# Performance work log

Hardware: AMD Instinct MI355X
Metric: run time of the kernel (lower is better)

## Reference

```python
import jax, jax.numpy as jnp
import numpy as np

G, P = 128, 32          # num scenes, peds per scene
H, E = 64, 64           # h_dim, embedding_dim_pooling
D1, D2 = 512, 1024      # mlp_pre_pool dims
EPS = 1e-5


def setup_inputs() -> dict:
    key = jax.random.key(0)
    ks = jax.random.split(key, 16)
    N = G * P
    starts = jnp.arange(G, dtype=jnp.int64) * P
    seq_start_end = jnp.stack([starts, starts + P], axis=1)
    def lin(k, fin, fout):
        kw, kb = jax.random.split(k)
        s = 1.0 / np.sqrt(fin)
        return (jax.random.uniform(kw, (fin, fout), jnp.float32, -s, s),
                jax.random.uniform(kb, (fout,), jnp.float32, -s, s))
    Ws, bs = lin(ks[0], 2, E)
    Wv, bv = lin(ks[1], 1, E)
    W1, b1 = lin(ks[2], 3 * E, D1)
    W2, b2 = lin(ks[3], D1, D2)
    return {
        "h_states": jax.random.normal(ks[4], (N, H), jnp.float32),
        "seq_start_end": seq_start_end,
        "end_pos": jax.random.normal(ks[5], (N, 2), jnp.float32),
        "end_pos_speed": jax.random.uniform(ks[6], (N, 1), jnp.float32),
        "Ws": Ws, "bs": bs, "Wv": Wv, "bv": bv,
        "W1": W1, "b1": b1, "g1": jnp.ones((D1,), jnp.float32), "be1": jnp.zeros((D1,), jnp.float32),
        "W2": W2, "b2": b2, "g2": jnp.ones((D2,), jnp.float32), "be2": jnp.zeros((D2,), jnp.float32),
    }


def _bn(h, gamma, beta):
    # BatchNorm1d in train mode, stats over the per-group edge batch (axes 1,2)
    m = h.mean(axis=(1, 2), keepdims=True)
    v = ((h - m) ** 2).mean(axis=(1, 2), keepdims=True)  # biased variance
    return (h - m) * jax.lax.rsqrt(v + EPS) * gamma + beta


def reference(h_states, seq_start_end, end_pos, end_pos_speed,
              Ws, bs, Wv, bv, W1, b1, g1, be1, W2, b2, g2, be2):
    g = seq_start_end.shape[0]
    p = h_states.shape[0] // g
    pos = end_pos.reshape(g, p, 2)
    spd = end_pos_speed.reshape(g, p, 1)
    hid = h_states.reshape(g, p, H)
    # edge (i, j): rel = pos[j] - pos[i]; features of j for hidden & speed
    rel = pos[:, None, :, :] - pos[:, :, None, :]          # [G,P(i),P(j),2]
    rel_e = rel @ Ws + bs                                   # [G,P,P,E]
    spd_e = spd @ Wv + bv                                   # [G,P,E]
    hid_b = jnp.broadcast_to(hid[:, None, :, :], (g, p, p, H))
    spd_b = jnp.broadcast_to(spd_e[:, None, :, :], (g, p, p, E))
    x = jnp.concatenate([rel_e, hid_b, spd_b], axis=-1)     # [G,P,P,3E]
    h1 = jax.nn.relu(_bn(x @ W1 + b1, g1, be1))             # [G,P,P,512]
    h2 = jax.nn.relu(_bn(h1 @ W2 + b2, g2, be2))            # [G,P,P,1024]
    pooled = h2.max(axis=2)                                 # max over j
    return pooled.reshape(g * p, -1)
```

## Files before the change

kernel.cpp:

```cpp
#include <hip/hip_runtime.h>
#include <cstdint>

typedef unsigned short ushort_t;
typedef __attribute__((ext_vector_type(8))) __bf16 bf16x8;
typedef __attribute__((ext_vector_type(4))) float f32x4;
typedef __attribute__((ext_vector_type(4))) int i32x4;

#define NG 128
#define NP 32
#define NH 64
#define ND1 512
#define ND2 1024

__device__ inline ushort_t f2bf(float f) {
    uint32_t u = __float_as_uint(f);
    uint32_t r = (u + 0x7FFFu + ((u >> 16) & 1u)) >> 16;
    return (ushort_t)r;
}

#define GLL16(gp, lp) __builtin_amdgcn_global_load_lds( \
    (const __attribute__((address_space(1))) unsigned int*)(gp), \
    (__attribute__((address_space(3))) unsigned int*)(lp), 16, 0, 0)

__global__ void k2_all(const float* __restrict__ hstates, const float* __restrict__ pos,
                       const float* __restrict__ spd, const float* __restrict__ W1,
                       const float* __restrict__ g1, const float* __restrict__ be1,
                       const float* __restrict__ Ws, const float* __restrict__ bs,
                       const float* __restrict__ Wv, const float* __restrict__ bv,
                       const float* __restrict__ b1, const float* __restrict__ W2,
                       ushort_t* __restrict__ W2T,
                       float* __restrict__ u1, float* __restrict__ w1,
                       float* __restrict__ psum) {
    __shared__ float hid_s[32][64];
    __shared__ float pos_s[32][2];
    __shared__ float spd_s[32];
    __shared__ ushort_t tile[64][65];
    int b = blockIdx.x, tid = threadIdx.x;
    if (b < 256) {
        int t0 = b * 256 + tid;
        #pragma unroll
        for (int z = 0; z < 4; z++) psum[t0 + z * 65536] = 0.f;
        int g = b >> 1;
        int ch = ((b & 1) << 8) + tid;
        for (int t = tid; t < 2048; t += 256) hid_s[t >> 6][t & 63] = hstates[g * 2048 + t];
        if (tid < 64) pos_s[tid >> 1][tid & 1] = pos[g * 64 + tid];
        if (tid < 32) spd_s[tid] = spd[g * 32 + tid];
        float m0 = 0.f, m1 = 0.f, uu = 0.f, vv = b1[ch];
        for (int e = 0; e < 64; e++) {
            float w1a = W1[e * ND1 + ch];
            float w1c = W1[(128 + e) * ND1 + ch];
            m0 += Ws[e] * w1a;
            m1 += Ws[64 + e] * w1a;
            uu += Wv[e] * w1c;
            vv += bs[e] * w1a + bv[e] * w1c;
        }
        __syncthreads();
        float cj[32], qj[32];
        #pragma unroll
        for (int j = 0; j < 32; j++) {
            qj[j] = pos_s[j][0] * m0 + pos_s[j][1] * m1;
            cj[j] = vv + spd_s[j] * uu;
        }
        for (int h = 0; h < 64; h++) {
            float w = W1[(64 + h) * ND1 + ch];
            #pragma unroll
            for (int j = 0; j < 32; j++) cj[j] += hid_s[j][h] * w;
        }
        float S1 = 0.f, S2 = 0.f, C1 = 0.f, Cq = 0.f, C2 = 0.f;
        #pragma unroll
        for (int j = 0; j < 32; j++) {
            S1 += qj[j]; S2 += qj[j] * qj[j];
            C1 += cj[j]; Cq += cj[j] * qj[j]; C2 += cj[j] * cj[j];
        }
        float mean = C1 * (1.0f / 32.0f);
        float sumsq = 64.f * S2 - 2.f * S1 * S1 + 64.f * Cq - 2.f * S1 * C1 + 32.f * C2;
        float var = sumsq * (1.0f / 1024.0f) - mean * mean;
        float A1 = rsqrtf(var + 1e-5f) * g1[ch];
        float B1 = be1[ch] - mean * A1;
        #pragma unroll
        for (int j = 0; j < 32; j++) {
            u1[(g * 32 + j) * ND1 + ch] = (qj[j] + cj[j]) * A1 + B1;
            w1[(g * 32 + j) * ND1 + ch] = qj[j] * A1;
        }
    } else {
        int tb = b - 256;
        int kb2 = tb & 7, nb = tb >> 3;
        #pragma unroll
        for (int e = 0; e < 16; e++) {
            int lin = tid + e * 256;
            int k = lin >> 6, n = lin & 63;
            tile[k][n] = f2bf(W2[(kb2 * 64 + k) * ND2 + nb * 64 + n]);
        }
        __syncthreads();
        #pragma unroll
        for (int e = 0; e < 16; e++) {
            int lin = tid + e * 256;
            int kl = lin & 63, nl = lin >> 6;
            int n = nb * 64 + nl, k = kb2 * 64 + kl;
            int idx = n * ND1 + ((k >> 6) << 6) + (((((k >> 3) & 7) ^ (n & 7))) << 3) + (k & 7);
            W2T[idx] = tile[kl][nl];
        }
    }
}

__global__ void k2b_h1(const float* __restrict__ u1c, const float* __restrict__ w1c,
                       ushort_t* __restrict__ h1) {
    int t = blockIdx.x * 256 + threadIdx.x;
    int k8 = t & 63;
    int row = t >> 6;
    int gc = row >> 10, rem = row & 1023;
    int i = rem >> 5, j = rem & 31;
    const float4* pu = reinterpret_cast<const float4*>(u1c + (size_t)(gc * 32 + j) * ND1 + k8 * 8);
    const float4* pw = reinterpret_cast<const float4*>(w1c + (size_t)(gc * 32 + i) * ND1 + k8 * 8);
    float4 ua = pu[0], ub = pu[1], wa = pw[0], wb = pw[1];
    uint32_t p0 = (uint32_t)f2bf(fmaxf(ua.x - wa.x, 0.f)) | ((uint32_t)f2bf(fmaxf(ua.y - wa.y, 0.f)) << 16);
    uint32_t p1 = (uint32_t)f2bf(fmaxf(ua.z - wa.z, 0.f)) | ((uint32_t)f2bf(fmaxf(ua.w - wa.w, 0.f)) << 16);
    uint32_t p2 = (uint32_t)f2bf(fmaxf(ub.x - wb.x, 0.f)) | ((uint32_t)f2bf(fmaxf(ub.y - wb.y, 0.f)) << 16);
    uint32_t p3 = (uint32_t)f2bf(fmaxf(ub.z - wb.z, 0.f)) | ((uint32_t)f2bf(fmaxf(ub.w - wb.w, 0.f)) << 16);
    i32x4 v = {(int)p0, (int)p1, (int)p2, (int)p3};
    int kt = k8 >> 3, c = k8 & 7;
    *reinterpret_cast<i32x4*>(h1 + (size_t)row * ND1 + (kt << 6) + (((c ^ (row & 7))) << 3)) = v;
}

__global__ __launch_bounds__(256, 2) void k3_gemm(
        const ushort_t* __restrict__ h1, const ushort_t* __restrict__ W2T,
        float* __restrict__ maxv, float* __restrict__ minv,
        float* __restrict__ psum, float* __restrict__ psq, int g0) {
    __shared__ __align__(16) ushort_t a_lds[128 * 64];
    __shared__ __align__(16) ushort_t b_lds[128 * 64];
    int b = blockIdx.x;
    int mt = (b & 7) + ((b >> 6) << 3);
    int nt = (b >> 3) & 7;
    int tid = threadIdx.x;
    int w = tid >> 6, l = tid & 63;
    int wm = w >> 1, wn = w & 1;
    int lo = l & 15, lhi = l >> 4;

    const char* Ag = reinterpret_cast<const char*>(h1) + (size_t)mt * 128 * ND1 * 2;
    const char* Bg = reinterpret_cast<const char*>(W2T) + (size_t)nt * 128 * ND1 * 2;
    int gbase = (w * 32 + (l >> 3)) * 1024 + (l & 7) * 16;
    char* aldsb = reinterpret_cast<char*>(a_lds) + w * 4096;
    char* bldsb = reinterpret_cast<char*>(b_lds) + w * 4096;

    f32x4 acc[4][4];
    #pragma unroll
    for (int a = 0; a < 4; a++)
        #pragma unroll
        for (int c = 0; c < 4; c++) acc[a][c] = (f32x4){0.f, 0.f, 0.f, 0.f};

    for (int kt = 0; kt < 8; kt++) {
        int kb = kt * 128;
        #pragma unroll
        for (int q = 0; q < 4; q++) {
            GLL16(Ag + gbase + q * 8192 + kb, aldsb + q * 1024);
            GLL16(Bg + gbase + q * 8192 + kb, bldsb + q * 1024);
        }
        __syncthreads();
        bf16x8 af[4][2], bfv[4][2];
        #pragma unroll
        for (int fr = 0; fr < 4; fr++) {
            int r = wm * 64 + fr * 16 + lo;
            #pragma unroll
            for (int kc = 0; kc < 2; kc++)
                af[fr][kc] = *reinterpret_cast<const bf16x8*>(
                    reinterpret_cast<const char*>(a_lds) + r * 128 + (((kc * 4 + lhi) ^ (r & 7)) << 4));
        }
        #pragma unroll
        for (int fc = 0; fc < 4; fc++) {
            int r = wn * 64 + fc * 16 + lo;
            #pragma unroll
            for (int kc = 0; kc < 2; kc++)
                bfv[fc][kc] = *reinterpret_cast<const bf16x8*>(
                    reinterpret_cast<const char*>(b_lds) + r * 128 + (((kc * 4 + lhi) ^ (r & 7)) << 4));
        }
        #pragma unroll
        for (int kc = 0; kc < 2; kc++)
            #pragma unroll
            for (int fr = 0; fr < 4; fr++)
                #pragma unroll
                for (int fc = 0; fc < 4; fc++)
                    acc[fr][fc] = __builtin_amdgcn_mfma_f32_16x16x32_bf16(af[fr][kc], bfv[fc][kc], acc[fr][fc], 0, 0, 0);
        __syncthreads();
    }

    int g = g0 + (mt >> 3);
    int ib = ((mt & 7) << 2) + wm * 2;
    #pragma unroll
    for (int fc = 0; fc < 4; fc++) {
        int col = nt * 128 + wn * 64 + fc * 16 + lo;
        float mx0 = -1e30f, mn0 = 1e30f, mx1 = -1e30f, mn1 = 1e30f, sm = 0.f, sq = 0.f;
        #pragma unroll
        for (int fr = 0; fr < 2; fr++)
            #pragma unroll
            for (int r = 0; r < 4; r++) {
                float y = acc[fr][fc][r];
                mx0 = fmaxf(mx0, y); mn0 = fminf(mn0, y);
                sm += y; sq += y * y;
            }
        #pragma unroll
        for (int fr = 2; fr < 4; fr++)
            #pragma unroll
            for (int r = 0; r < 4; r++) {
                float y = acc[fr][fc][r];
                mx1 = fmaxf(mx1, y); mn1 = fminf(mn1, y);
                sm += y; sq += y * y;
            }
        #pragma unroll
        for (int mask = 16; mask < 64; mask <<= 1) {
            mx0 = fmaxf(mx0, __shfl_xor(mx0, mask, 64));
            mn0 = fminf(mn0, __shfl_xor(mn0, mask, 64));
            mx1 = fmaxf(mx1, __shfl_xor(mx1, mask, 64));
            mn1 = fminf(mn1, __shfl_xor(mn1, mask, 64));
            sm += __shfl_xor(sm, mask, 64);
            sq += __shfl_xor(sq, mask, 64);
        }
        if (lhi == 0) {
            size_t i0 = (size_t)(g * 32 + ib) * ND2 + col;
            maxv[i0] = mx0; minv[i0] = mn0;
            maxv[i0 + ND2] = mx1; minv[i0 + ND2] = mn1;
            atomicAdd(&psum[g * ND2 + col], sm);
            atomicAdd(&psq[g * ND2 + col], sq);
        }
    }
}

__global__ void k4_final(const float* __restrict__ maxv, const float* __restrict__ minv,
                         const float* __restrict__ psum, const float* __restrict__ psq,
                         const float* __restrict__ b2, const float* __restrict__ g2,
                         const float* __restrict__ be2, float* __restrict__ out) {
    int g = blockIdx.x >> 2;
    int col = ((blockIdx.x & 3) << 8) + threadIdx.x;
    float b2v = b2[col];
    float s = psum[g * ND2 + col] * (1.f / 1024.f);
    float q = psq[g * ND2 + col] * (1.f / 1024.f);
    float mean = s + b2v;
    float var = q + 2.f * b2v * s + b2v * b2v - mean * mean;
    float A2 = rsqrtf(var + 1e-5f) * g2[col];
    float B2 = be2[col] - mean * A2;
    for (int i = 0; i < 32; i++) {
        size_t idx = (size_t)(g * 32 + i) * ND2 + col;
        float y = ((A2 >= 0.f) ? maxv[idx] : minv[idx]) + b2v;
        out[idx] = fmaxf(y * A2 + B2, 0.f);
    }
}

extern "C" void kernel_launch(void* const* d_in, const int* in_sizes, int n_in,
                              void* d_out, int out_size, void* d_ws, size_t ws_size,
                              hipStream_t stream) {
    (void)in_sizes; (void)n_in; (void)out_size;
    const float* h_states = (const float*)d_in[0];
    const float* end_pos  = (const float*)d_in[2];
    const float* end_spd  = (const float*)d_in[3];
    const float* Ws  = (const float*)d_in[4];
    const float* bs  = (const float*)d_in[5];
    const float* Wv  = (const float*)d_in[6];
    const float* bv  = (const float*)d_in[7];
    const float* W1  = (const float*)d_in[8];
    const float* b1  = (const float*)d_in[9];
    const float* g1  = (const float*)d_in[10];
    const float* be1 = (const float*)d_in[11];
    const float* W2  = (const float*)d_in[12];
    const float* b2  = (const float*)d_in[13];
    const float* g2  = (const float*)d_in[14];
    const float* be2 = (const float*)d_in[15];
    float* ws = (float*)d_ws;
    float* u1   = ws + 2048;
    float* w1x  = ws + 2099200;
    ushort_t* W2T = (ushort_t*)(ws + 4196352);
    float* maxv = ws + 4458496;
    float* minv = ws + 8652800;
    float* psum = ws + 12847104;
    float* psq  = ws + 12978176;
    ushort_t* h1 = (ushort_t*)(ws + 13109248);
    float* out = (float*)d_out;

    const size_t fixed_f = 13109248ULL;
    int CG = 128;
    while (CG > 4 && (fixed_f + (size_t)CG * 262144ULL) * 4ULL > ws_size) CG >>= 1;
    int nch = 128 / CG;

    hipLaunchKernelGGL(k2_all, dim3(384), dim3(256), 0, stream,
                       h_states, end_pos, end_spd, W1, g1, be1,
                       Ws, bs, Wv, bv, b1, W2, W2T, u1, w1x, psum);
    for (int c = 0; c < nch; c++) {
        const float* u1c = u1 + (size_t)c * CG * 32 * ND1;
        const float* w1c = w1x + (size_t)c * CG * 32 * ND1;
        hipLaunchKernelGGL(k2b_h1, dim3(CG * 256), dim3(256), 0, stream, u1c, w1c, h1);
        hipLaunchKernelGGL(k3_gemm, dim3(CG * 64), dim3(256), 0, stream,
                           h1, W2T, maxv, minv, psum, psq, c * CG);
    }
    hipLaunchKernelGGL(k4_final, dim3(512), dim3(256), 0, stream,
                       maxv, minv, psum, psq, b2, g2, be2, out);
}
```

Measured before the change: 325.1 us.

## Rewrite W2 GEMM as 256x256 double-buffered 8-wave pipeline with XCD-aware block order

Each k3_gemm block now computes a 256x256 tile with 512 threads instead of 128x128 with 256. It uses a 128KB LDS double buffer, so global-to-LDS loads for the next K step are issued between MFMA phases, with explicit barriers, vmcnt waits and setprio around the MFMA bursts. Block IDs are also remapped so consecutive blocks are spread across XCDs. The intent is to raise arithmetic intensity and hide memory latency behind MFMA work. The cost is the large LDS footprint, which limits occupancy, plus a fragile hand-written schedule.

```diff
diff --git a/kernel.cpp b/kernel.cpp
--- a/kernel.cpp
+++ b/kernel.cpp
@@ -122,102 +122,160 @@
     *reinterpret_cast<i32x4*>(h1 + (size_t)row * ND1 + (kt << 6) + (((c ^ (row & 7))) << 3)) = v;
 }
 
-__global__ __launch_bounds__(256, 2) void k3_gemm(
+#define BARX() do { __builtin_amdgcn_sched_barrier(0); __builtin_amdgcn_s_barrier(); __builtin_amdgcn_sched_barrier(0); } while (0)
+#define STG(XG, XL, kt, h) do { \
+    const char* _g = (XG) + (size_t)(h) * 131072 + (size_t)(kt) * 128; \
+    char* _l = (XL) + (((kt) & 1) << 15) + ((h) << 14) + ldsw; \
+    GLL16(_g, _l); \
+    GLL16(_g + 65536, _l + 8192); \
+} while (0)
+
+__global__ __launch_bounds__(512, 2) void k3_gemm(
         const ushort_t* __restrict__ h1, const ushort_t* __restrict__ W2T,
         float* __restrict__ maxv, float* __restrict__ minv,
-        float* __restrict__ psum, float* __restrict__ psq, int g0) {
-    __shared__ __align__(16) ushort_t a_lds[128 * 64];
-    __shared__ __align__(16) ushort_t b_lds[128 * 64];
+        float* __restrict__ psum, float* __restrict__ psq, int g0, int nwg8) {
+    __shared__ __align__(16) char lds[131072];
     int b = blockIdx.x;
-    int mt = (b & 7) + ((b >> 6) << 3);
-    int nt = (b >> 3) & 7;
+    int orig = (b & 7) * nwg8 + (b >> 3);
+    int mt = orig >> 2, nt = orig & 3;
     int tid = threadIdx.x;
     int w = tid >> 6, l = tid & 63;
-    int wm = w >> 1, wn = w & 1;
+    int wm = w >> 2, wn = w & 3;
     int lo = l & 15, lhi = l >> 4;
 
-    const char* Ag = reinterpret_cast<const char*>(h1) + (size_t)mt * 128 * ND1 * 2;
-    const char* Bg = reinterpret_cast<const char*>(W2T) + (size_t)nt * 128 * ND1 * 2;
-    int gbase = (w * 32 + (l >> 3)) * 1024 + (l & 7) * 16;
-    char* aldsb = reinterpret_cast<char*>(a_lds) + w * 4096;
-    char* bldsb = reinterpret_cast<char*>(b_lds) + w * 4096;
-
-    f32x4 acc[4][4];
+    int srow = w * 8 + (l >> 3);
+    int sbyte = (l & 7) * 16;
+    const char* Agb = reinterpret_cast<const char*>(h1) + (size_t)(mt * 256 + srow) * 1024 + sbyte;
+    const char* Bgb = reinterpret_cast<const char*>(W2T) + (size_t)(nt * 256 + srow) * 1024 + sbyte;
+    char* ldsA = lds;
+    char* ldsB = lds + 65536;
+    int ldsw = w * 1024;
+
+    int csw0 = ((lhi) ^ (lo & 7)) << 4;
+    int csw1 = ((4 + lhi) ^ (lo & 7)) << 4;
+    const char* aRB = ldsA + wm * 16384 + lo * 128;
+    const char* bRB = ldsB + (wn >> 1) * 16384 + ((wn & 1) * 64 + lo) * 128;
+
+    f32x4 acc[8][4];
     #pragma unroll
-    for (int a = 0; a < 4; a++)
-        #pragma unroll
-        for (int c = 0; c < 4; c++) acc[a][c] = (f32x4){0.f, 0.f, 0.f, 0.f};
-
-    for (int kt = 0; kt < 8; kt++) {
-        int kb = kt * 128;
-        #pragma unroll
-        for (int q = 0; q < 4; q++) {
-            GLL16(Ag + gbase + q * 8192 + kb, aldsb + q * 1024);
-            GLL16(Bg + gbase + q * 8192 + kb, bldsb + q * 1024);
-        }
-        __syncthreads();
-        bf16x8 af[4][2], bfv[4][2];
-        #pragma unroll
-        for (int fr = 0; fr < 4; fr++) {
-            int r = wm * 64 + fr * 16 + lo;
-            #pragma unroll
-            for (int kc = 0; kc < 2; kc++)
-                af[fr][kc] = *reinterpret_cast<const bf16x8*>(
-                    reinterpret_cast<const char*>(a_lds) + r * 128 + (((kc * 4 + lhi) ^ (r & 7)) << 4));
-        }
-        #pragma unroll
-        for (int fc = 0; fc < 4; fc++) {
-            int r = wn * 64 + fc * 16 + lo;
-            #pragma unroll
-            for (int kc = 0; kc < 2; kc++)
-                bfv[fc][kc] = *reinterpret_cast<const bf16x8*>(
-                    reinterpret_cast<const char*>(b_lds) + r * 128 + (((kc * 4 + lhi) ^ (r & 7)) << 4));
-        }
+    for (int x = 0; x < 8; x++)
+        #pragma unroll
+        for (int y = 0; y < 4; y++) acc[x][y] = (f32x4){0.f, 0.f, 0.f, 0.f};
+
+    bf16x8 a0[4][2], a1[4][2], bb0[2][2], bb1[2][2];
+
+    auto rdA = [&](bf16x8 (&ar)[4][2], int slot, int qm) {
+        #pragma unroll
+        for (int f = 0; f < 4; f++) {
+            ar[f][0] = *reinterpret_cast<const bf16x8*>(aRB + slot * 32768 + (qm * 64 + f * 16) * 128 + csw0);
+            ar[f][1] = *reinterpret_cast<const bf16x8*>(aRB + slot * 32768 + (qm * 64 + f * 16) * 128 + csw1);
+        }
+    };
+    auto rdB = [&](bf16x8 (&br)[2][2], int slot, int qn) {
+        #pragma unroll
+        for (int f = 0; f < 2; f++) {
+            br[f][0] = *reinterpret_cast<const bf16x8*>(bRB + slot * 32768 + (qn * 2 + f) * 2048 + csw0);
+            br[f][1] = *reinterpret_cast<const bf16x8*>(bRB + slot * 32768 + (qn * 2 + f) * 2048 + csw1);
+        }
+    };
+    auto mm = [&](int fr0, int fc0, bf16x8 (&ar)[4][2], bf16x8 (&br)[2][2]) {
+        __builtin_amdgcn_s_setprio(1);
         #pragma unroll
         for (int kc = 0; kc < 2; kc++)
             #pragma unroll
-            for (int fr = 0; fr < 4; fr++)
+            for (int f = 0; f < 4; f++)
                 #pragma unroll
-                for (int fc = 0; fc < 4; fc++)
-                    acc[fr][fc] = __builtin_amdgcn_mfma_f32_16x16x32_bf16(af[fr][kc], bfv[fc][kc], acc[fr][fc], 0, 0, 0);
-        __syncthreads();
-    }
-
-    int g = g0 + (mt >> 3);
-    int ib = ((mt & 7) << 2) + wm * 2;
+                for (int c = 0; c < 2; c++)
+                    acc[fr0 + f][fc0 + c] = __builtin_amdgcn_mfma_f32_16x16x32_bf16(
+                        ar[f][kc], br[c][kc], acc[fr0 + f][fc0 + c], 0, 0, 0);
+        __builtin_amdgcn_s_setprio(0);
+    };
+
+    STG(Agb, ldsA, 0, 0); STG(Agb, ldsA, 0, 1);
+    STG(Bgb, ldsB, 0, 0); STG(Bgb, ldsB, 0, 1);
+    STG(Agb, ldsA, 1, 0); STG(Agb, ldsA, 1, 1);
+    STG(Bgb, ldsB, 1, 0); STG(Bgb, ldsB, 1, 1);
+    asm volatile("s_waitcnt vmcnt(8)" ::: "memory");
+    BARX();
+
+    for (int J = 0; J < 4; J++) {
+        int kB1 = 2 * J + 1;
+        rdA(a0, 0, 0); rdB(bb0, 0, 0);
+        if (J > 0) STG(Agb, ldsA, kB1, 0);
+        BARX();
+        mm(0, 0, a0, bb0);
+        BARX();
+        rdB(bb1, 0, 1);
+        if (J > 0) STG(Agb, ldsA, kB1, 1);
+        BARX();
+        mm(0, 2, a0, bb1);
+        BARX();
+        rdA(a1, 0, 1);
+        if (J < 3) STG(Bgb, ldsB, kB1 + 1, 0);
+        BARX();
+        mm(4, 0, a1, bb0);
+        BARX();
+        if (J < 3) STG(Bgb, ldsB, kB1 + 1, 1);
+        BARX();
+        mm(4, 2, a1, bb1);
+        if (J < 3) asm volatile("s_waitcnt vmcnt(4)" ::: "memory");
+        else       asm volatile("s_waitcnt vmcnt(0)" ::: "memory");
+        BARX();
+        rdA(a0, 1, 0); rdB(bb0, 1, 0);
+        if (J < 3) STG(Agb, ldsA, kB1 + 1, 0);
+        BARX();
+        mm(0, 0, a0, bb0);
+        BARX();
+        rdB(bb1, 1, 1);
+        if (J < 3) STG(Agb, ldsA, kB1 + 1, 1);
+        BARX();
+        mm(0, 2, a0, bb1);
+        BARX();
+        rdA(a1, 1, 1);
+        if (J < 3) STG(Bgb, ldsB, kB1 + 2, 0);
+        BARX();
+        mm(4, 0, a1, bb0);
+        BARX();
+        if (J < 3) STG(Bgb, ldsB, kB1 + 2, 1);
+        BARX();
+        mm(4, 2, a1, bb1);
+        if (J < 3) asm volatile("s_waitcnt vmcnt(4)" ::: "memory");
+        BARX();
+    }
+
+    int g = g0 + (mt >> 2);
+    int qq = mt & 3;
     #pragma unroll
     for (int fc = 0; fc < 4; fc++) {
-        int col = nt * 128 + wn * 64 + fc * 16 + lo;
-        float mx0 = -1e30f, mn0 = 1e30f, mx1 = -1e30f, mn1 = 1e30f, sm = 0.f, sq = 0.f;
-        #pragma unroll
-        for (int fr = 0; fr < 2; fr++)
+        int col = nt * 256 + wn * 64 + fc * 16 + lo;
+        float sm = 0.f, sq = 0.f;
+        float mx[4], mn[4];
+        #pragma unroll
+        for (int m = 0; m < 4; m++) {
+            float vmx = -1e30f, vmn = 1e30f;
             #pragma unroll
-            for (int r = 0; r < 4; r++) {
-                float y = acc[fr][fc][r];
-                mx0 = fmaxf(mx0, y); mn0 = fminf(mn0, y);
-                sm += y; sq += y * y;
+            for (int fh = 0; fh < 2; fh++)
+                #pragma unroll
+                for (int r = 0; r < 4; r++) {
+                    float y = acc[2 * m + fh][fc][r];
+                    vmx = fmaxf(vmx, y); vmn = fminf(vmn, y);
+                    sm += y; sq += y * y;
+                }
+            vmx = fmaxf(vmx, __shfl_xor(vmx, 16, 64));
+            vmx = fmaxf(vmx, __shfl_xor(vmx, 32, 64));
+            vmn = fminf(vmn, __shfl_xor(vmn, 16, 64));
+            vmn = fminf(vmn, __shfl_xor(vmn, 32, 64));
+            mx[m] = vmx; mn[m] = vmn;
+        }
+        sm += __shfl_xor(sm, 16, 64); sm += __shfl_xor(sm, 32, 64);
+        sq += __shfl_xor(sq, 16, 64); sq += __shfl_xor(sq, 32, 64);
+        if (lhi == 0) {
+            #pragma unroll
+            for (int m = 0; m < 4; m++) {
+                int i = qq * 8 + wm * 4 + m;
+                size_t idx = (size_t)(g * 32 + i) * ND2 + col;
+                maxv[idx] = mx[m]; minv[idx] = mn[m];
             }
-        #pragma unroll
-        for (int fr = 2; fr < 4; fr++)
-            #pragma unroll
-            for (int r = 0; r < 4; r++) {
-                float y = acc[fr][fc][r];
-                mx1 = fmaxf(mx1, y); mn1 = fminf(mn1, y);
-                sm += y; sq += y * y;
-            }
-        #pragma unroll
-        for (int mask = 16; mask < 64; mask <<= 1) {
-            mx0 = fmaxf(mx0, __shfl_xor(mx0, mask, 64));
-            mn0 = fminf(mn0, __shfl_xor(mn0, mask, 64));
-            mx1 = fmaxf(mx1, __shfl_xor(mx1, mask, 64));
-            mn1 = fminf(mn1, __shfl_xor(mn1, mask, 64));
-            sm += __shfl_xor(sm, mask, 64);
-            sq += __shfl_xor(sq, mask, 64);
-        }
-        if (lhi == 0) {
-            size_t i0 = (size_t)(g * 32 + ib) * ND2 + col;
-            maxv[i0] = mx0; minv[i0] = mn0;
-            maxv[i0 + ND2] = mx1; minv[i0 + ND2] = mn1;
             atomicAdd(&psum[g * ND2 + col], sm);
             atomicAdd(&psq[g * ND2 + col], sq);
         }
@@ -286,8 +344,8 @@
         const float* u1c = u1 + (size_t)c * CG * 32 * ND1;
         const float* w1c = w1x + (size_t)c * CG * 32 * ND1;
         hipLaunchKernelGGL(k2b_h1, dim3(CG * 256), dim3(256), 0, stream, u1c, w1c, h1);
-        hipLaunchKernelGGL(k3_gemm, dim3(CG * 64), dim3(256), 0, stream,
-                           h1, W2T, maxv, minv, psum, psq, c * CG);
+        hipLaunchKernelGGL(k3_gemm, dim3(CG * 16), dim3(512), 0, stream,
+                           h1, W2T, maxv, minv, psum, psq, c * CG, CG * 2);
     }
     hipLaunchKernelGGL(k4_final, dim3(512), dim3(256), 0, stream,
                        maxv, minv, psum, psq, b2, g2, be2, out);
```

Measured after the change: 306.3 us. 1.06x faster.
